# Performance work log

Hardware: AMD Instinct MI355X
Metric: run time of the kernel (lower is better)

Reference implementation:

```python
import jax, jax.numpy as jnp
import numpy as np

B, S, D, H = 8, 1024, 1024, 16
HD = D // H  # head_size = 64


def layernorm(x, g, b, eps=1e-5):
    mu = jnp.mean(x, axis=-1, keepdims=True)
    var = jnp.var(x, axis=-1, keepdims=True)
    return (x - mu) * jax.lax.rsqrt(var + eps) * g + b


def setup_inputs() -> dict:
    key = jax.random.key(0)
    ks = jax.random.split(key, 12)
    s_attn = 1.0 / np.sqrt(D)
    inp = {
        "x": jax.random.normal(ks[0], (B, S, D), dtype=jnp.float32),
        # per-head q/k/v projections (bias=False), stacked: [H, D, HD]
        "Wq": jax.random.normal(ks[1], (H, D, HD), dtype=jnp.float32) * s_attn,
        "Wk": jax.random.normal(ks[2], (H, D, HD), dtype=jnp.float32) * s_attn,
        "Wv": jax.random.normal(ks[3], (H, D, HD), dtype=jnp.float32) * s_attn,
        "Wo": jax.random.normal(ks[4], (D, D), dtype=jnp.float32) * s_attn,
        "bo": jnp.zeros((D,), dtype=jnp.float32),
        # FFN: hidden = 1 * n_embd (as in source)
        "W1": jax.random.normal(ks[5], (D, D), dtype=jnp.float32) * s_attn,
        "b1": jnp.zeros((D,), dtype=jnp.float32),
        "W2": jax.random.normal(ks[6], (D, D), dtype=jnp.float32) * s_attn,
        "b2": jnp.zeros((D,), dtype=jnp.float32),
        "g_ln1": jnp.ones((D,), dtype=jnp.float32),
        "b_ln1": jnp.zeros((D,), dtype=jnp.float32),
        "g_ln2": jnp.ones((D,), dtype=jnp.float32),
        "b_ln2": jnp.zeros((D,), dtype=jnp.float32),
    }
    return inp


def reference(x, Wq, Wk, Wv, Wo, bo, W1, b1, W2, b2, g_ln1, b_ln1, g_ln2, b_ln2):
    # pre-LN self-attention
    h = layernorm(x, g_ln1, b_ln1)
    q = jnp.einsum("bsd,hde->bhse", h, Wq)
    k = jnp.einsum("bsd,hde->bhse", h, Wk)
    v = jnp.einsum("bsd,hde->bhse", h, Wv)
    scale = HD ** -0.5  # k.shape[-1] ** -0.5
    wei = jax.nn.softmax(jnp.einsum("bhse,bhte->bhst", q, k) * scale, axis=-1)
    attn = jnp.einsum("bhst,bhte->bhse", wei, v)  # [B,H,S,HD]
    # concat heads (head order matches torch.cat over head list)
    attn = attn.transpose(0, 2, 1, 3).reshape(B, S, D)
    sa = attn @ Wo + bo
    x = x + sa
    # pre-LN FFN with exact GELU (torch nn.GELU default)
    h2 = layernorm(x, g_ln2, b_ln2)
    ff = jax.nn.gelu(h2 @ W1 + b1, approximate=False) @ W2 + b2
    return x + ff
```

## Files before the change

### kernel.cpp

```cpp
#include <hip/hip_runtime.h>
#include <hip/hip_bf16.h>
#include <math.h>

#define B_ 8
#define S_ 1024
#define D_ 1024
#define H_ 16
#define HD_ 64

typedef __bf16 bf16x8 __attribute__((ext_vector_type(8)));
typedef __bf16 bf16x4 __attribute__((ext_vector_type(4)));
typedef float f32x4 __attribute__((ext_vector_type(4)));

#define FMAX3(a, b, c) fmaxf(fmaxf((a), (b)), (c))

__device__ __forceinline__ void gld_lds16(const __bf16* g, __bf16* l) {
  __builtin_amdgcn_global_load_lds(
      (const __attribute__((address_space(1))) void*)g,
      (__attribute__((address_space(3))) void*)l, 16, 0, 0);
}

__global__ __launch_bounds__(256) void prep(const float* __restrict__ x,
                                            const float* __restrict__ g,
                                            const float* __restrict__ b,
                                            __bf16* __restrict__ h_out,
                                            const float* __restrict__ Wq,
                                            const float* __restrict__ Wk,
                                            const float* __restrict__ Wv,
                                            const float* __restrict__ Wo,
                                            const float* __restrict__ W1,
                                            const float* __restrict__ W2,
                                            __bf16* __restrict__ wt) {
  __shared__ float t[64][65];
  const int bid = blockIdx.x;
  const int tid = threadIdx.x;

  if (bid < 8192) {
    float* red = &t[0][0];
    const float* xr = x + (size_t)bid * D_;
    __bf16* outr = h_out + (size_t)bid * D_;

    float4 v = ((const float4*)xr)[tid];
    float s = v.x + v.y + v.z + v.w;
    float ss = v.x * v.x + v.y * v.y + v.z * v.z + v.w * v.w;

    #pragma unroll
    for (int m = 1; m < 64; m <<= 1) {
      s += __shfl_xor(s, m);
      ss += __shfl_xor(ss, m);
    }
    int wid = tid >> 6;
    if ((tid & 63) == 0) { red[wid] = s; red[4 + wid] = ss; }
    __syncthreads();
    if (tid == 0) {
      float ts = red[0] + red[1] + red[2] + red[3];
      float tss = red[4] + red[5] + red[6] + red[7];
      float mu = ts * (1.0f / D_);
      float var = tss * (1.0f / D_) - mu * mu;
      red[8] = mu;
      red[9] = rsqrtf(var + 1e-5f);
    }
    __syncthreads();
    float mu = red[8], rstd = red[9];
    float4 gv = ((const float4*)g)[tid];
    float4 bv = ((const float4*)b)[tid];
    bf16x4 o;
    o[0] = (__bf16)((v.x - mu) * rstd * gv.x + bv.x);
    o[1] = (__bf16)((v.y - mu) * rstd * gv.y + bv.y);
    o[2] = (__bf16)((v.z - mu) * rstd * gv.z + bv.z);
    o[3] = (__bf16)((v.w - mu) * rstd * gv.w + bv.w);
    *(bf16x4*)(outr + tid * 4) = o;
    return;
  }

  const int tt = bid - 8192;
  const int z = tt >> 8;
  const int y = (tt >> 4) & 15;
  const int xx = tt & 15;
  const int r = tid >> 4, c4 = (tid & 15) * 4;

  const float* src;
  int stride, orowbase, kbase;
  if (z < 3) {
    const float* W = (z == 0 ? Wq : z == 1 ? Wk : Wv);
    src = W + (size_t)y * (D_ * HD_) + (size_t)(xx * 64) * HD_;
    stride = HD_;
    orowbase = z * 1024 + y * 64;
    kbase = xx * 64;
  } else {
    const float* W = (z == 3 ? Wo : z == 4 ? W1 : W2);
    src = W + (size_t)(y * 64) * D_ + xx * 64;
    stride = D_;
    orowbase = z * 1024 + xx * 64;
    kbase = y * 64;
  }

  #pragma unroll
  for (int i = 0; i < 4; ++i) {
    float4 v = *(const float4*)&src[(size_t)(i * 16 + r) * stride + c4];
    t[i * 16 + r][c4 + 0] = v.x;
    t[i * 16 + r][c4 + 1] = v.y;
    t[i * 16 + r][c4 + 2] = v.z;
    t[i * 16 + r][c4 + 3] = v.w;
  }
  __syncthreads();
  #pragma unroll
  for (int i = 0; i < 4; ++i) {
    bf16x4 o;
    #pragma unroll
    for (int j = 0; j < 4; ++j) o[j] = (__bf16)t[c4 + j][i * 16 + r];
    *(bf16x4*)&wt[(size_t)(orowbase + i * 16 + r) * 1024 + kbase + c4] = o;
  }
}

__global__ __launch_bounds__(256) void ln_bf16(const __bf16* __restrict__ x,
                                               const float* __restrict__ g,
                                               const float* __restrict__ b,
                                               __bf16* __restrict__ out) {
  int row = blockIdx.x;
  const __bf16* xr = x + (size_t)row * D_;
  __bf16* outr = out + (size_t)row * D_;
  int tid = threadIdx.x;

  bf16x4 xv = *(const bf16x4*)(xr + tid * 4);
  float v0 = (float)xv[0], v1 = (float)xv[1], v2 = (float)xv[2], v3 = (float)xv[3];
  float s = v0 + v1 + v2 + v3;
  float ss = v0 * v0 + v1 * v1 + v2 * v2 + v3 * v3;

  #pragma unroll
  for (int m = 1; m < 64; m <<= 1) {
    s += __shfl_xor(s, m);
    ss += __shfl_xor(ss, m);
  }
  __shared__ float red[10];
  int wid = tid >> 6;
  if ((tid & 63) == 0) { red[wid] = s; red[4 + wid] = ss; }
  __syncthreads();
  if (tid == 0) {
    float ts = red[0] + red[1] + red[2] + red[3];
    float tss = red[4] + red[5] + red[6] + red[7];
    float mu = ts * (1.0f / D_);
    float var = tss * (1.0f / D_) - mu * mu;
    red[8] = mu;
    red[9] = rsqrtf(var + 1e-5f);
  }
  __syncthreads();
  float mu = red[8], rstd = red[9];
  float4 gv = ((const float4*)g)[tid];
  float4 bv = ((const float4*)b)[tid];
  bf16x4 o;
  o[0] = (__bf16)((v0 - mu) * rstd * gv.x + bv.x);
  o[1] = (__bf16)((v1 - mu) * rstd * gv.y + bv.y);
  o[2] = (__bf16)((v2 - mu) * rstd * gv.z + bv.z);
  o[3] = (__bf16)((v3 - mu) * rstd * gv.w + bv.w);
  *(bf16x4*)(outr + tid * 4) = o;
}

#define MODE_QKV 0
#define MODE_PROJ 1
#define MODE_FF1 2
#define MODE_FF2 3

#define QSCALE 0.18033688011112042f

__device__ __forceinline__ float gelu_tanh(float v) {
  float u = 0.7978845608028654f * v * (1.0f + 0.044715f * v * v);
  float e = __builtin_amdgcn_exp2f(2.885390081777927f * u);
  float th = 1.0f - 2.0f * __builtin_amdgcn_rcpf(e + 1.0f);
  return 0.5f * v * (1.0f + th);
}

template <int MODE>
__global__ __launch_bounds__(256) void gemm_mfma(const __bf16* __restrict__ A,
                                                 const __bf16* __restrict__ Bt,
                                                 const float* __restrict__ bias,
                                                 const float* __restrict__ residf,
                                                 const __bf16* __restrict__ residb,
                                                 float* __restrict__ outf,
                                                 __bf16* __restrict__ outb,
                                                 int M, int N, int K) {
  __shared__ __align__(16) __bf16 As[2][128 * 64];
  __shared__ __align__(16) __bf16 Bs[2][128 * 64];
  const int tid = threadIdx.x;

  const int gx = (int)gridDim.x;
  const int nwg = gx * (int)gridDim.y;
  const int flat = (int)blockIdx.y * gx + (int)blockIdx.x;
  const int wg = (flat & 7) * (nwg >> 3) + (flat >> 3);
  const int m0 = (wg / gx) * 128, n0 = (wg % gx) * 128;

  const int w = tid >> 6, l = tid & 63, lr = l & 15, lg = l >> 4;
  const int wm = (w >> 1) * 64, wn = (w & 1) * 64;

  f32x4 acc[4][4] = {};

  auto stage = [&](int buf, int k0) {
    #pragma unroll
    for (int i = 0; i < 4; ++i) {
      int e = i * 256 + tid;
      int row = e >> 3;
      int col = ((e & 7) ^ (row & 7)) * 8;
      gld_lds16(A + (size_t)(m0 + row) * K + k0 + col, &As[buf][e * 8]);
    }
    #pragma unroll
    for (int i = 0; i < 4; ++i) {
      int e = i * 256 + tid;
      int row = e >> 3;
      int col = ((e & 7) ^ (row & 7)) * 8;
      gld_lds16(Bt + (size_t)(n0 + row) * K + k0 + col, &Bs[buf][e * 8]);
    }
  };

  auto compute = [&](int buf) {
    #pragma unroll
    for (int kk = 0; kk < 2; ++kk) {
      bf16x8 af[4], bfr[4];
      #pragma unroll
      for (int i = 0; i < 4; ++i)
        af[i] = *(const bf16x8*)
            &As[buf][((wm + i * 16 + lr) * 8 + ((kk * 4 + lg) ^ (lr & 7))) * 8];
      #pragma unroll
      for (int j = 0; j < 4; ++j)
        bfr[j] = *(const bf16x8*)
            &Bs[buf][((wn + j * 16 + lr) * 8 + ((kk * 4 + lg) ^ (lr & 7))) * 8];
      #pragma unroll
      for (int i = 0; i < 4; ++i)
        #pragma unroll
        for (int j = 0; j < 4; ++j)
          acc[i][j] = __builtin_amdgcn_mfma_f32_16x16x32_bf16(af[i], bfr[j], acc[i][j], 0, 0, 0);
    }
  };

  const int NT = K >> 6;
  stage(0, 0);

  for (int t = 0; t < NT; ++t) {
    const int buf = t & 1;
    const int tn = (t + 1 < NT) ? (t + 1) : (NT - 1);
    stage(buf ^ 1, tn * 64);
    asm volatile("s_waitcnt vmcnt(8)" ::: "memory");
    __builtin_amdgcn_sched_barrier(0);
    __builtin_amdgcn_s_barrier();
    __builtin_amdgcn_sched_barrier(0);
    compute(buf);
    __builtin_amdgcn_s_barrier();
  }

  #pragma unroll
  for (int i = 0; i < 4; ++i) {
    #pragma unroll
    for (int j = 0; j < 4; ++j) {
      #pragma unroll
      for (int r = 0; r < 4; ++r) {
        int m = m0 + wm + i * 16 + 4 * lg + r;
        int n = n0 + wn + j * 16 + lr;
        float val = acc[i][j][r];
        if (MODE == MODE_QKV) {
          int b = m >> 10, s = m & 1023;
          int which = n >> 10, hh = (n >> 6) & 15, e = n & 63;
          if (which == 0) val *= QSCALE;
          outb[(size_t)which * 8388608 + ((size_t)(b * 16 + hh) * 1024 + s) * 64 + e] =
              (__bf16)val;
        } else if (MODE == MODE_PROJ) {
          size_t idx = (size_t)m * 1024 + n;
          outb[idx] = (__bf16)(residf[idx] + val + bias[n]);
        } else if (MODE == MODE_FF1) {
          outb[(size_t)m * 1024 + n] = (__bf16)gelu_tanh(val + bias[n]);
        } else {
          size_t idx = (size_t)m * 1024 + n;
          outf[idx] = (float)residb[idx] + val + bias[n];
        }
      }
    }
  }
}

__global__ __launch_bounds__(512) void fattn(const __bf16* __restrict__ q,
                                             const __bf16* __restrict__ k,
                                             const __bf16* __restrict__ v,
                                             __bf16* __restrict__ outC) {
  __shared__ __align__(16) __bf16 Klds[2][64 * 64];
  __shared__ __align__(16) __bf16 Vp[2][64 * 64];

  const int bid = blockIdx.x;
  const int bh = (bid & 7) * 16 + ((bid >> 3) & 15);
  const int qt = bid >> 7;
  const int tid = threadIdx.x;
  const int w = tid >> 6, l = tid & 63;
  const int lr = l & 15, lg = l >> 4;

  const size_t base = (size_t)bh * (S_ * HD_);
  const int qrow0 = qt * 128 + w * 16;
  const __bf16* kg = k + base;
  const __bf16* vg = v + base;

  const int krow = tid >> 3;
  const int kcol = ((tid & 7) ^ (krow & 7)) * 8;
  const int vc = (l & 0x20) + ((l & 0xC) << 1) + ((l & 0x10) >> 2) + (l & 3);
  const int vchi = vc >> 3, vclo = vc & 7;

  bf16x8 qf0, qf1;
  {
    const __bf16* qp = q + base + (size_t)(qrow0 + lr) * HD_ + lg * 8;
    qf0 = *(const bf16x8*)(qp);
    qf1 = *(const bf16x8*)(qp + 32);
  }

  const __bf16 onev = (lr == 0) ? (__bf16)1.0f : (__bf16)0.0f;
  const bf16x8 vones = {onev, onev, onev, onev, onev, onev, onev, onev};

  f32x4 oacc[5] = {};
  float m_run = -1e30f;

  gld_lds16(kg + (size_t)krow * HD_ + kcol, &Klds[0][tid * 8]);
  bf16x8 vr;
  {
    vr = *(const bf16x8*)(vg + (size_t)l * HD_ + w * 8);
    #pragma unroll
    for (int i = 0; i < 8; ++i)
      Vp[0][(w * 8 + i) * 64 + ((vchi ^ i) << 3) + vclo] = vr[i];
    vr = *(const bf16x8*)(vg + (size_t)(64 + l) * HD_ + w * 8);
  }
  asm volatile("s_waitcnt vmcnt(1) lgkmcnt(0)" ::: "memory");
  __builtin_amdgcn_sched_barrier(0);
  __builtin_amdgcn_s_barrier();
  __builtin_amdgcn_sched_barrier(0);

  int cur = 0;
  for (int t = 0; t < 16; ++t) {
    {
      int tn = (t < 15) ? (t + 1) : 15;
      gld_lds16(kg + ((size_t)tn * 64 + krow) * HD_ + kcol, &Klds[cur ^ 1][tid * 8]);
    }

    f32x4 sacc[4];
    const __bf16* kb = &Klds[cur][0];
    #pragma unroll
    for (int g = 0; g < 4; ++g) {
      bf16x8 kf0 = *(const bf16x8*)&kb[((16 * g + lr) * 8 + (lg ^ (lr & 7))) * 8];
      bf16x8 kf1 = *(const bf16x8*)&kb[((16 * g + lr) * 8 + ((lg + 4) ^ (lr & 7))) * 8];
      f32x4 z = {0.f, 0.f, 0.f, 0.f};
      z = __builtin_amdgcn_mfma_f32_16x16x32_bf16(kf0, qf0, z, 0, 0, 0);
      sacc[g] = __builtin_amdgcn_mfma_f32_16x16x32_bf16(kf1, qf1, z, 0, 0, 0);
    }

    #pragma unroll
    for (int i = 0; i < 8; ++i)
      Vp[cur ^ 1][(w * 8 + i) * 64 + ((vchi ^ i) << 3) + vclo] = vr[i];
    {
      int tnn = (t < 14) ? (t + 2) : 15;
      vr = *(const bf16x8*)(vg + ((size_t)tnn * 64 + l) * HD_ + w * 8);
    }

    float m0 = FMAX3(sacc[0][0], sacc[0][1], sacc[0][2]);
    float m1 = FMAX3(sacc[0][3], sacc[1][0], sacc[1][1]);
    float m2 = FMAX3(sacc[1][2], sacc[1][3], sacc[2][0]);
    float m3 = FMAX3(sacc[2][1], sacc[2][2], sacc[2][3]);
    float m4 = FMAX3(sacc[3][0], sacc[3][1], sacc[3][2]);
    float tm = FMAX3(FMAX3(m0, m1, m2), FMAX3(m3, m4, sacc[3][3]), m_run);
    tm = fmaxf(tm, __shfl_xor(tm, 16));
    tm = fmaxf(tm, __shfl_xor(tm, 32));

    if (!__all(tm - m_run <= 11.5f)) {
      float corr = __builtin_amdgcn_exp2f(m_run - tm);
      m_run = tm;
      #pragma unroll
      for (int r = 0; r < 4; ++r) {
        float cq = __shfl(corr, 4 * lg + r);
        #pragma unroll
        for (int g = 0; g < 5; ++g) oacc[g][r] *= cq;
      }
    }

    float p[4][4];
    #pragma unroll
    for (int g = 0; g < 4; ++g)
      #pragma unroll
      for (int r = 0; r < 4; ++r)
        p[g][r] = __builtin_amdgcn_exp2f(sacc[g][r] - m_run);

    bf16x8 af0, af1;
    #pragma unroll
    for (int j = 0; j < 8; ++j) {
      af0[j] = (__bf16)p[j >> 2][j & 3];
      af1[j] = (__bf16)p[2 + (j >> 2)][j & 3];
    }
    #pragma unroll
    for (int g = 0; g < 4; ++g) {
      bf16x8 vf0 = *(const bf16x8*)&Vp[cur][(16 * g + lr) * 64 + ((lg ^ (lr & 7)) << 3)];
      bf16x8 vf1 = *(const bf16x8*)&Vp[cur][(16 * g + lr) * 64 + (((lg + 4) ^ (lr & 7)) << 3)];
      oacc[g] = __builtin_amdgcn_mfma_f32_16x16x32_bf16(af0, vf0, oacc[g], 0, 0, 0);
      oacc[g] = __builtin_amdgcn_mfma_f32_16x16x32_bf16(af1, vf1, oacc[g], 0, 0, 0);
    }
    oacc[4] = __builtin_amdgcn_mfma_f32_16x16x32_bf16(af0, vones, oacc[4], 0, 0, 0);
    oacc[4] = __builtin_amdgcn_mfma_f32_16x16x32_bf16(af1, vones, oacc[4], 0, 0, 0);

    asm volatile("s_waitcnt vmcnt(1) lgkmcnt(0)" ::: "memory");
    __builtin_amdgcn_sched_barrier(0);
    __builtin_amdgcn_s_barrier();
    __builtin_amdgcn_sched_barrier(0);
    cur ^= 1;
  }

  const int b = bh >> 4, hh = bh & 15;
  #pragma unroll
  for (int r = 0; r < 4; ++r) {
    float linv = 1.0f / __shfl(oacc[4][r], l & 48);
    int srow = qrow0 + 4 * lg + r;
    __bf16* op = outC + ((size_t)(b * S_ + srow)) * D_ + hh * HD_;
    #pragma unroll
    for (int g = 0; g < 4; ++g) op[16 * g + lr] = (__bf16)(oacc[g][r] * linv);
  }
}

extern "C" void kernel_launch(void* const* d_in, const int* in_sizes, int n_in,
                              void* d_out, int out_size, void* d_ws, size_t ws_size,
                              hipStream_t stream) {
  const float* x   = (const float*)d_in[0];
  const float* Wq  = (const float*)d_in[1];
  const float* Wk  = (const float*)d_in[2];
  const float* Wv  = (const float*)d_in[3];
  const float* Wo  = (const float*)d_in[4];
  const float* bo  = (const float*)d_in[5];
  const float* W1  = (const float*)d_in[6];
  const float* b1  = (const float*)d_in[7];
  const float* W2  = (const float*)d_in[8];
  const float* b2  = (const float*)d_in[9];
  const float* g1  = (const float*)d_in[10];
  const float* bl1 = (const float*)d_in[11];
  const float* g2  = (const float*)d_in[12];
  const float* bl2 = (const float*)d_in[13];
  float* out = (float*)d_out;

  const size_t MN = (size_t)B_ * S_ * D_;
  __bf16* h     = (__bf16*)d_ws;
  __bf16* wt    = h + MN;
  __bf16* qkv   = wt + (size_t)6144 * 1024;
  __bf16* attnC = qkv + 3 * MN;
  __bf16* ff1   = attnC + MN;
  __bf16* mid   = ff1 + MN;

  __bf16* wqkv_t = wt;
  __bf16* wo_t   = wt + (size_t)3072 * 1024;
  __bf16* w1_t   = wt + (size_t)4096 * 1024;
  __bf16* w2_t   = wt + (size_t)5120 * 1024;

  const int rows = B_ * S_;

  prep<<<rows + 1536, 256, 0, stream>>>(x, g1, bl1, h, Wq, Wk, Wv, Wo, W1, W2, wt);

  gemm_mfma<MODE_QKV><<<dim3(24, 64), 256, 0, stream>>>(
      h, wqkv_t, nullptr, nullptr, nullptr, nullptr, qkv, rows, 3072, D_);
  fattn<<<1024, 512, 0, stream>>>(qkv, qkv + MN, qkv + 2 * MN, attnC);
  gemm_mfma<MODE_PROJ><<<dim3(8, 64), 256, 0, stream>>>(
      attnC, wo_t, bo, x, nullptr, nullptr, mid, rows, D_, D_);
  ln_bf16<<<rows, 256, 0, stream>>>(mid, g2, bl2, h);
  gemm_mfma<MODE_FF1><<<dim3(8, 64), 256, 0, stream>>>(
      h, w1_t, b1, nullptr, nullptr, nullptr, ff1, rows, D_, D_);
  gemm_mfma<MODE_FF2><<<dim3(8, 64), 256, 0, stream>>>(
      ff1, w2_t, b2, nullptr, mid, out, nullptr, rows, D_, D_);
}
```

Baseline: 218.9 us.

## Process two 16-row query tiles per wave in flash attention

Each wave in the attention kernel now handles 32 query rows as two independent 16-row tiles sharing the same K and V fragments from LDS, and the grid is halved. This amortizes K/V global-to-LDS staging and LDS fragment reads over twice as many queries. In exchange, register pressure roughly doubles for accumulators and scores, and there are half as many blocks to fill the GPU.

After: 217.2 us. No clear change (-0.8%).

```diff
diff --git a/kernel.cpp b/kernel.cpp
--- a/kernel.cpp
+++ b/kernel.cpp
@@ -290,7 +290,7 @@
   const int lr = l & 15, lg = l >> 4;
 
   const size_t base = (size_t)bh * (S_ * HD_);
-  const int qrow0 = qt * 128 + w * 16;
+  const int qrow0 = qt * 256 + w * 32;
   const __bf16* kg = k + base;
   const __bf16* vg = v + base;
 
@@ -299,18 +299,21 @@
   const int vc = (l & 0x20) + ((l & 0xC) << 1) + ((l & 0x10) >> 2) + (l & 3);
   const int vchi = vc >> 3, vclo = vc & 7;
 
-  bf16x8 qf0, qf1;
+  bf16x8 qfA0, qfA1, qfB0, qfB1;
   {
     const __bf16* qp = q + base + (size_t)(qrow0 + lr) * HD_ + lg * 8;
-    qf0 = *(const bf16x8*)(qp);
-    qf1 = *(const bf16x8*)(qp + 32);
+    qfA0 = *(const bf16x8*)(qp);
+    qfA1 = *(const bf16x8*)(qp + 32);
+    const __bf16* qpB = qp + (size_t)16 * HD_;
+    qfB0 = *(const bf16x8*)(qpB);
+    qfB1 = *(const bf16x8*)(qpB + 32);
   }
 
   const __bf16 onev = (lr == 0) ? (__bf16)1.0f : (__bf16)0.0f;
   const bf16x8 vones = {onev, onev, onev, onev, onev, onev, onev, onev};
 
-  f32x4 oacc[5] = {};
-  float m_run = -1e30f;
+  f32x4 oaccA[5] = {}, oaccB[5] = {};
+  float mA = -1e30f, mB = -1e30f;
 
   gld_lds16(kg + (size_t)krow * HD_ + kcol, &Klds[0][tid * 8]);
   bf16x8 vr;
@@ -333,15 +336,18 @@
       gld_lds16(kg + ((size_t)tn * 64 + krow) * HD_ + kcol, &Klds[cur ^ 1][tid * 8]);
     }
 
-    f32x4 sacc[4];
+    f32x4 sA[4], sB[4];
     const __bf16* kb = &Klds[cur][0];
     #pragma unroll
     for (int g = 0; g < 4; ++g) {
       bf16x8 kf0 = *(const bf16x8*)&kb[((16 * g + lr) * 8 + (lg ^ (lr & 7))) * 8];
       bf16x8 kf1 = *(const bf16x8*)&kb[((16 * g + lr) * 8 + ((lg + 4) ^ (lr & 7))) * 8];
       f32x4 z = {0.f, 0.f, 0.f, 0.f};
-      z = __builtin_amdgcn_mfma_f32_16x16x32_bf16(kf0, qf0, z, 0, 0, 0);
-      sacc[g] = __builtin_amdgcn_mfma_f32_16x16x32_bf16(kf1, qf1, z, 0, 0, 0);
+      z = __builtin_amdgcn_mfma_f32_16x16x32_bf16(kf0, qfA0, z, 0, 0, 0);
+      sA[g] = __builtin_amdgcn_mfma_f32_16x16x32_bf16(kf1, qfA1, z, 0, 0, 0);
+      f32x4 zb = {0.f, 0.f, 0.f, 0.f};
+      zb = __builtin_amdgcn_mfma_f32_16x16x32_bf16(kf0, qfB0, zb, 0, 0, 0);
+      sB[g] = __builtin_amdgcn_mfma_f32_16x16x32_bf16(kf1, qfB1, zb, 0, 0, 0);
     }
 
     #pragma unroll
@@ -352,48 +358,85 @@
       vr = *(const bf16x8*)(vg + ((size_t)tnn * 64 + l) * HD_ + w * 8);
     }
 
-    float m0 = FMAX3(sacc[0][0], sacc[0][1], sacc[0][2]);
-    float m1 = FMAX3(sacc[0][3], sacc[1][0], sacc[1][1]);
-    float m2 = FMAX3(sacc[1][2], sacc[1][3], sacc[2][0]);
-    float m3 = FMAX3(sacc[2][1], sacc[2][2], sacc[2][3]);
-    float m4 = FMAX3(sacc[3][0], sacc[3][1], sacc[3][2]);
-    float tm = FMAX3(FMAX3(m0, m1, m2), FMAX3(m3, m4, sacc[3][3]), m_run);
-    tm = fmaxf(tm, __shfl_xor(tm, 16));
-    tm = fmaxf(tm, __shfl_xor(tm, 32));
-
-    if (!__all(tm - m_run <= 11.5f)) {
-      float corr = __builtin_amdgcn_exp2f(m_run - tm);
-      m_run = tm;
-      #pragma unroll
-      for (int r = 0; r < 4; ++r) {
-        float cq = __shfl(corr, 4 * lg + r);
+    bf16x8 afA0, afA1;
+    {
+      float m0 = FMAX3(sA[0][0], sA[0][1], sA[0][2]);
+      float m1 = FMAX3(sA[0][3], sA[1][0], sA[1][1]);
+      float m2 = FMAX3(sA[1][2], sA[1][3], sA[2][0]);
+      float m3 = FMAX3(sA[2][1], sA[2][2], sA[2][3]);
+      float m4 = FMAX3(sA[3][0], sA[3][1], sA[3][2]);
+      float tm = FMAX3(FMAX3(m0, m1, m2), FMAX3(m3, m4, sA[3][3]), mA);
+      tm = fmaxf(tm, __shfl_xor(tm, 16));
+      tm = fmaxf(tm, __shfl_xor(tm, 32));
+      if (!__all(tm - mA <= 11.5f)) {
+        float corr = __builtin_amdgcn_exp2f(mA - tm);
+        mA = tm;
         #pragma unroll
-        for (int g = 0; g < 5; ++g) oacc[g][r] *= cq;
+        for (int r = 0; r < 4; ++r) {
+          float cq = __shfl(corr, 4 * lg + r);
+          #pragma unroll
+          for (int g = 0; g < 5; ++g) oaccA[g][r] *= cq;
+        }
       }
-    }
-
-    float p[4][4];
-    #pragma unroll
-    for (int g = 0; g < 4; ++g)
-      #pragma unroll
-      for (int r = 0; r < 4; ++r)
-        p[g][r] = __builtin_amdgcn_exp2f(sacc[g][r] - m_run);
-
-    bf16x8 af0, af1;
-    #pragma unroll
-    for (int j = 0; j < 8; ++j) {
-      af0[j] = (__bf16)p[j >> 2][j & 3];
-      af1[j] = (__bf16)p[2 + (j >> 2)][j & 3];
-    }
+      float p[4][4];
+      #pragma unroll
+      for (int g = 0; g < 4; ++g)
+        #pragma unroll
+        for (int r = 0; r < 4; ++r)
+          p[g][r] = __builtin_amdgcn_exp2f(sA[g][r] - mA);
+      #pragma unroll
+      for (int j = 0; j < 8; ++j) {
+        afA0[j] = (__bf16)p[j >> 2][j & 3];
+        afA1[j] = (__bf16)p[2 + (j >> 2)][j & 3];
+      }
+    }
+
+    bf16x8 afB0, afB1;
+    {
+      float m0 = FMAX3(sB[0][0], sB[0][1], sB[0][2]);
+      float m1 = FMAX3(sB[0][3], sB[1][0], sB[1][1]);
+      float m2 = FMAX3(sB[1][2], sB[1][3], sB[2][0]);
+      float m3 = FMAX3(sB[2][1], sB[2][2], sB[2][3]);
+      float m4 = FMAX3(sB[3][0], sB[3][1], sB[3][2]);
+      float tm = FMAX3(FMAX3(m0, m1, m2), FMAX3(m3, m4, sB[3][3]), mB);
+      tm = fmaxf(tm, __shfl_xor(tm, 16));
+      tm = fmaxf(tm, __shfl_xor(tm, 32));
+      if (!__all(tm - mB <= 11.5f)) {
+        float corr = __builtin_amdgcn_exp2f(mB - tm);
+        mB = tm;
+        #pragma unroll
+        for (int r = 0; r < 4; ++r) {
+          float cq = __shfl(corr, 4 * lg + r);
+          #pragma unroll
+          for (int g = 0; g < 5; ++g) oaccB[g][r] *= cq;
+        }
+      }
+      float p[4][4];
+      #pragma unroll
+      for (int g = 0; g < 4; ++g)
+        #pragma unroll
+        for (int r = 0; r < 4; ++r)
+          p[g][r] = __builtin_amdgcn_exp2f(sB[g][r] - mB);
+      #pragma unroll
+      for (int j = 0; j < 8; ++j) {
+        afB0[j] = (__bf16)p[j >> 2][j & 3];
+        afB1[j] = (__bf16)p[2 + (j >> 2)][j & 3];
+      }
+    }
+
     #pragma unroll
     for (int g = 0; g < 4; ++g) {
       bf16x8 vf0 = *(const bf16x8*)&Vp[cur][(16 * g + lr) * 64 + ((lg ^ (lr & 7)) << 3)];
       bf16x8 vf1 = *(const bf16x8*)&Vp[cur][(16 * g + lr) * 64 + (((lg + 4) ^ (lr & 7)) << 3)];
-      oacc[g] = __builtin_amdgcn_mfma_f32_16x16x32_bf16(af0, vf0, oacc[g], 0, 0, 0);
-      oacc[g] = __builtin_amdgcn_mfma_f32_16x16x32_bf16(af1, vf1, oacc[g], 0, 0, 0);
-    }
-    oacc[4] = __builtin_amdgcn_mfma_f32_16x16x32_bf16(af0, vones, oacc[4], 0, 0, 0);
-    oacc[4] = __builtin_amdgcn_mfma_f32_16x16x32_bf16(af1, vones, oacc[4], 0, 0, 0);
+      oaccA[g] = __builtin_amdgcn_mfma_f32_16x16x32_bf16(afA0, vf0, oaccA[g], 0, 0, 0);
+      oaccA[g] = __builtin_amdgcn_mfma_f32_16x16x32_bf16(afA1, vf1, oaccA[g], 0, 0, 0);
+      oaccB[g] = __builtin_amdgcn_mfma_f32_16x16x32_bf16(afB0, vf0, oaccB[g], 0, 0, 0);
+      oaccB[g] = __builtin_amdgcn_mfma_f32_16x16x32_bf16(afB1, vf1, oaccB[g], 0, 0, 0);
+    }
+    oaccA[4] = __builtin_amdgcn_mfma_f32_16x16x32_bf16(afA0, vones, oaccA[4], 0, 0, 0);
+    oaccA[4] = __builtin_amdgcn_mfma_f32_16x16x32_bf16(afA1, vones, oaccA[4], 0, 0, 0);
+    oaccB[4] = __builtin_amdgcn_mfma_f32_16x16x32_bf16(afB0, vones, oaccB[4], 0, 0, 0);
+    oaccB[4] = __builtin_amdgcn_mfma_f32_16x16x32_bf16(afB1, vones, oaccB[4], 0, 0, 0);
 
     asm volatile("s_waitcnt vmcnt(1) lgkmcnt(0)" ::: "memory");
     __builtin_amdgcn_sched_barrier(0);
@@ -405,11 +448,16 @@
   const int b = bh >> 4, hh = bh & 15;
   #pragma unroll
   for (int r = 0; r < 4; ++r) {
-    float linv = 1.0f / __shfl(oacc[4][r], l & 48);
-    int srow = qrow0 + 4 * lg + r;
-    __bf16* op = outC + ((size_t)(b * S_ + srow)) * D_ + hh * HD_;
-    #pragma unroll
-    for (int g = 0; g < 4; ++g) op[16 * g + lr] = (__bf16)(oacc[g][r] * linv);
+    float linvA = 1.0f / __shfl(oaccA[4][r], l & 48);
+    float linvB = 1.0f / __shfl(oaccB[4][r], l & 48);
+    int srowA = qrow0 + 4 * lg + r;
+    __bf16* opA = outC + ((size_t)(b * S_ + srowA)) * D_ + hh * HD_;
+    __bf16* opB = opA + (size_t)16 * D_;
+    #pragma unroll
+    for (int g = 0; g < 4; ++g) {
+      opA[16 * g + lr] = (__bf16)(oaccA[g][r] * linvA);
+      opB[16 * g + lr] = (__bf16)(oaccB[g][r] * linvB);
+    }
   }
 }
 
@@ -451,7 +499,7 @@
 
   gemm_mfma<MODE_QKV><<<dim3(24, 64), 256, 0, stream>>>(
       h, wqkv_t, nullptr, nullptr, nullptr, nullptr, qkv, rows, 3072, D_);
-  fattn<<<1024, 512, 0, stream>>>(qkv, qkv + MN, qkv + 2 * MN, attnC);
+  fattn<<<512, 512, 0, stream>>>(qkv, qkv + MN, qkv + 2 * MN, attnC);
   gemm_mfma<MODE_PROJ><<<dim3(8, 64), 256, 0, stream>>>(
       attnC, wo_t, bo, x, nullptr, nullptr, mid, rows, D_, D_);
   ln_bf16<<<rows, 256, 0, stream>>>(mid, g2, bl2, h);
```
